# Kernel tuning notes

Hardware: AMD Instinct MI355X
Metric: run time of the kernel (lower is better)

Reference implementation:

```python
import jax, jax.numpy as jnp
import numpy as np

N_CELLS = 100000
CHANNELS = 64
NNZ = 1600000


def _spmm(rows, cols, vals, x, n):
    # y[i] = sum_{k: rows[k]==i} vals[k] * x[cols[k]]  -- sparse Laplacian matvec over features
    return jax.ops.segment_sum(vals[:, None] * x[cols], rows, num_segments=n)


def setup_inputs() -> dict:
    key = jax.random.key(0)
    ks = jax.random.split(key, 9)
    scale = 1.0 / np.sqrt(CHANNELS)
    return {
        "x": jax.random.normal(ks[0], (N_CELLS, CHANNELS), dtype=jnp.float32),
        "down_rows": jax.random.randint(ks[1], (NNZ,), 0, N_CELLS, dtype=jnp.int32),
        "down_cols": jax.random.randint(ks[2], (NNZ,), 0, N_CELLS, dtype=jnp.int32),
        "down_vals": jax.random.normal(ks[3], (NNZ,), dtype=jnp.float32),
        "up_rows": jax.random.randint(ks[4], (NNZ,), 0, N_CELLS, dtype=jnp.int32),
        "up_cols": jax.random.randint(ks[5], (NNZ,), 0, N_CELLS, dtype=jnp.int32),
        "up_vals": jax.random.normal(ks[6], (NNZ,), dtype=jnp.float32),
        "w_conv": jax.random.normal(ks[7], (CHANNELS, CHANNELS), dtype=jnp.float32) * scale,
        "w_lin": jax.random.normal(ks[8], (CHANNELS, CHANNELS), dtype=jnp.float32) * scale,
    }


def reference(x, down_rows, down_cols, down_vals, up_rows, up_cols, up_vals, w_conv, w_lin):
    n = x.shape[0]
    xw = x @ w_conv  # shared Conv weight for both Laplacian paths
    x_down = _spmm(down_rows, down_cols, down_vals, xw, n)  # L_down @ (x W_conv)
    x_up = _spmm(up_rows, up_cols, up_vals, xw, n)          # L_up   @ (x W_conv)
    x_id = x @ w_lin                                         # bias-free Linear
    # Aggregation(update_func='sigmoid'): sum messages then activate
    return jax.nn.sigmoid(x_down + x_up + x_id)
```

## Files before the change

kernel.cpp:

```cpp
#include <hip/hip_runtime.h>
#include <hip/hip_bf16.h>
#include <hip/hip_fp16.h>

#define CH 64
#define RPB 128
#define RPB_SH 7
#define MAXNB 800
#define NGRP 8
#define SUBCAP 600
#define CAPG (NGRP * SUBCAP)
#define BATCH 3072
#define SPILLMAX 16384
#define FILL_BLOCKS 521
#define GEMM_PHYS 503
#define NVB (GEMM_PHYS * 2)

typedef __attribute__((ext_vector_type(8))) _Float16 half8;
typedef __attribute__((ext_vector_type(4))) float f32x4;

#define COLOFF_MASK 0x00FFFF80

__global__ __launch_bounds__(512) void gemm_fill_kernel(
    const float* __restrict__ x, const float* __restrict__ wc,
    const float* __restrict__ wl, __half* __restrict__ xwh,
    float* __restrict__ out, int n,
    const int* __restrict__ r1, const int* __restrict__ c1, const float* __restrict__ v1,
    const int* __restrict__ r2, const int* __restrict__ c2, const float* __restrict__ v2,
    int* __restrict__ gcur, int* __restrict__ spillcnt, int4* __restrict__ spill,
    int2* __restrict__ ebuf, int nnz, int nb) {
  __shared__ int2 stash[BATCH];
  __shared__ unsigned short sbuck[BATCH];
  __shared__ int hist[MAXNB];
  __shared__ int rbase[MAXNB];

  const int tid = threadIdx.x;

  if (blockIdx.x < (unsigned)FILL_BLOCKS) {
    const int grp = (int)(blockIdx.x & (NGRP - 1));
    const int tot = 2 * nnz;
    const int nbatches = (tot + BATCH - 1) / BATCH;
    for (int bt = blockIdx.x; bt < nbatches; bt += FILL_BLOCKS) {
      for (int i = tid; i < nb; i += 512) hist[i] = 0;
      __syncthreads();

      const int e0 = bt * BATCH;
      const int m = min(BATCH, tot - e0);
      for (int i = tid; i < m; i += 512) {
        const int e = e0 + i;
        int r, c;
        float v;
        if (e < nnz) {
          r = r1[e]; c = c1[e]; v = v1[e];
        } else {
          r = r2[e - nnz]; c = c2[e - nnz]; v = v2[e - nnz];
        }
        const int b = r >> RPB_SH;
        stash[i] = make_int2(((r & (RPB - 1)) << 24) | (c << 7), __float_as_int(v));
        sbuck[i] = (unsigned short)b;
        atomicAdd(&hist[b], 1);
      }
      __syncthreads();

      for (int b = tid; b < nb; b += 512) {
        const int c = hist[b];
        rbase[b] = c ? atomicAdd(&gcur[grp * nb + b], c) : 0;
        hist[b] = 0;
      }
      __syncthreads();

      for (int i = tid; i < m; i += 512) {
        const int b = sbuck[i];
        const int2 rec = stash[i];
        const int p = rbase[b] + atomicAdd(&hist[b], 1);
        if (p < SUBCAP) {
          ebuf[(size_t)b * CAPG + grp * SUBCAP + p] = rec;
        } else {
          const int sp = atomicAdd(spillcnt, 1);
          if (sp < SPILLMAX)
            spill[sp] = make_int4(b * RPB + (rec.x >> 24), rec.x & COLOFF_MASK,
                                  rec.y, 0);
        }
      }
      __syncthreads();
    }
    return;
  }

  const int vb = (int)(blockIdx.x - FILL_BLOCKS) * 2 + (tid >> 8);
  const int t256 = tid & 255;
  const int lane = t256 & 63;
  const int wv = t256 >> 6;
  const int mat = wv >> 1;
  const int tile = wv & 1;
  const float* __restrict__ W = mat ? wl : wc;

  const int i16 = lane & 15;
  const int kseg = lane >> 4;

  half8 bhi[4][2], blo[4][2];
#pragma unroll
  for (int nt = 0; nt < 4; ++nt)
#pragma unroll
    for (int kk = 0; kk < 2; ++kk)
#pragma unroll
      for (int j = 0; j < 8; ++j) {
        const float w = W[(kk * 32 + kseg * 8 + j) * CH + nt * 16 + i16];
        const _Float16 hh = (_Float16)w;
        bhi[nt][kk][j] = hh;
        blo[nt][kk][j] = (_Float16)(w - (float)hh);
      }

  const int ngroups = (n + 31) >> 5;
  for (int g = vb; g < ngroups; g += NVB) {
    const int base = g * 32 + tile * 16;
    const int row = base + i16;
    const int rowc = (row < n) ? row : (n - 1);
    const float* xp = x + (size_t)rowc * CH + kseg * 8;

    float af[16];
    {
      const float4 p0 = *(const float4*)(xp);
      const float4 p1 = *(const float4*)(xp + 4);
      const float4 q0 = *(const float4*)(xp + 32);
      const float4 q1 = *(const float4*)(xp + 36);
      af[0] = p0.x; af[1] = p0.y; af[2] = p0.z; af[3] = p0.w;
      af[4] = p1.x; af[5] = p1.y; af[6] = p1.z; af[7] = p1.w;
      af[8] = q0.x; af[9] = q0.y; af[10] = q0.z; af[11] = q0.w;
      af[12] = q1.x; af[13] = q1.y; af[14] = q1.z; af[15] = q1.w;
    }
    half8 ahi[2], alo[2];
#pragma unroll
    for (int kk = 0; kk < 2; ++kk)
#pragma unroll
      for (int j = 0; j < 8; ++j) {
        const float f = af[kk * 8 + j];
        const _Float16 hh = (_Float16)f;
        ahi[kk][j] = hh;
        alo[kk][j] = (_Float16)(f - (float)hh);
      }

    f32x4 acc[4];
#pragma unroll
    for (int nt = 0; nt < 4; ++nt) {
      f32x4 a = {0.f, 0.f, 0.f, 0.f};
#pragma unroll
      for (int kk = 0; kk < 2; ++kk) {
        a = __builtin_amdgcn_mfma_f32_16x16x32_f16(ahi[kk], bhi[nt][kk], a, 0, 0, 0);
        a = __builtin_amdgcn_mfma_f32_16x16x32_f16(alo[kk], bhi[nt][kk], a, 0, 0, 0);
        a = __builtin_amdgcn_mfma_f32_16x16x32_f16(ahi[kk], blo[nt][kk], a, 0, 0, 0);
      }
      acc[nt] = a;
    }

    if (mat == 0) {
#pragma unroll
      for (int nt = 0; nt < 4; ++nt)
#pragma unroll
        for (int r = 0; r < 4; ++r) {
          const int orow = base + kseg * 4 + r;
          if (orow < n)
            xwh[(size_t)orow * CH + nt * 16 + i16] = __float2half(acc[nt][r]);
        }
    } else {
#pragma unroll
      for (int nt = 0; nt < 4; ++nt)
#pragma unroll
        for (int r = 0; r < 4; ++r) {
          const int orow = base + kseg * 4 + r;
          if (orow < n)
            out[(size_t)orow * CH + nt * 16 + i16] = acc[nt][r];
        }
    }
  }
}

union U8 {
  uint4 u4;
  __half h[8];
};

__device__ __forceinline__ void edge_fma(float* a, const U8& u, float v) {
#pragma unroll
  for (int k = 0; k < 8; ++k)
    a[k] = fmaf(v, __half2float(u.h[k]), a[k]);
}

#define PERG 2

__global__ __launch_bounds__(512, 8) void sortgather2_kernel(
    const int* __restrict__ gcur, const int2* __restrict__ ebuf,
    const char* __restrict__ xwbytes, float4* __restrict__ outf4,
    const int* __restrict__ spillcnt, const int4* __restrict__ spill,
    int n, int nb) {
  __shared__ int2 raw[CAPG];
  __shared__ int hist[RPB];
  __shared__ int rowstart[RPB];
  __shared__ int cur[RPB];
  const int tid = threadIdx.x;
  const int b = blockIdx.x;
  const int beg = b * CAPG;

  if (tid < RPB) hist[tid] = 0;
  __syncthreads();

  int2 myrec[NGRP * PERG];
#pragma unroll
  for (int g = 0; g < NGRP; ++g) {
    const int cg = min(gcur[g * nb + b], SUBCAP);
#pragma unroll
    for (int j = 0; j < PERG; ++j) {
      const int i = j * 512 + tid;
      const bool ok = i < cg;
      int2 rec = ok ? ebuf[beg + g * SUBCAP + i] : make_int2(-1, 0);
      myrec[g * PERG + j] = rec;
      if (ok) atomicAdd(&hist[rec.x >> 24], 1);
    }
  }
  __syncthreads();

  int v = 0;
  if (tid < RPB) {
    v = hist[tid];
    cur[tid] = v;
  }
  __syncthreads();
  for (int off = 1; off < RPB; off <<= 1) {
    int t = 0;
    if (tid < RPB && tid >= off) t = cur[tid - off];
    __syncthreads();
    if (tid < RPB) cur[tid] += t;
    __syncthreads();
  }
  if (tid < RPB) {
    rowstart[tid] = cur[tid] - v;
    cur[tid] = cur[tid] - v;
  }
  __syncthreads();

#pragma unroll
  for (int g = 0; g < NGRP; ++g)
#pragma unroll
    for (int j = 0; j < PERG; ++j) {
      const int2 rec = myrec[g * PERG + j];
      if (rec.x >= 0) {
        const int pos = atomicAdd(&cur[rec.x >> 24], 1);
        raw[pos] = rec;
      }
    }
  __syncthreads();

  const int lane = tid & 63;
  const int g8 = lane >> 3;
  const int l8 = lane & 7;
  const int l8b = l8 << 4;
  const int wv = tid >> 6;
  const int sc = min(*spillcnt, SPILLMAX);

  for (int rl = wv; rl < RPB; rl += 8) {
    const int row = b * RPB + rl;
    if (row >= n) continue;

    float a[8];
#pragma unroll
    for (int k = 0; k < 8; ++k) a[k] = 0.f;

    const int rbeg = rowstart[rl];
    const int rend = rbeg + hist[rl];

    int e = rbeg;
    for (; e + 32 <= rend; e += 32) {
      int2 rc[4];
      U8 u[4];
#pragma unroll
      for (int q = 0; q < 4; ++q) rc[q] = raw[e + q * 8 + g8];
#pragma unroll
      for (int q = 0; q < 4; ++q)
        u[q].u4 = *(const uint4*)(xwbytes + (rc[q].x & COLOFF_MASK) + l8b);
#pragma unroll
      for (int q = 0; q < 4; ++q) edge_fma(a, u[q], __int_as_float(rc[q].y));
    }
    for (; e + 16 <= rend; e += 16) {
      const int2 rc0 = raw[e + g8];
      const int2 rc1 = raw[e + 8 + g8];
      U8 u0, u1;
      u0.u4 = *(const uint4*)(xwbytes + (rc0.x & COLOFF_MASK) + l8b);
      u1.u4 = *(const uint4*)(xwbytes + (rc1.x & COLOFF_MASK) + l8b);
      edge_fma(a, u0, __int_as_float(rc0.y));
      edge_fma(a, u1, __int_as_float(rc1.y));
    }
    for (; e < rend; e += 8) {
      const int idx = e + g8;
      const bool ok = idx < rend;
      const int2 rc = raw[ok ? idx : (rend - 1)];
      U8 u;
      u.u4 = *(const uint4*)(xwbytes + (rc.x & COLOFF_MASK) + l8b);
      edge_fma(a, u, ok ? __int_as_float(rc.y) : 0.f);
    }

    if (sc > 0) {
      for (int s = 0; s < sc; ++s) {
        const int4 r = spill[s];
        if (r.x == row && g8 == 0) {
          U8 u;
          u.u4 = *(const uint4*)(xwbytes + r.y + l8b);
          edge_fma(a, u, __int_as_float(r.z));
        }
      }
    }

#pragma unroll
    for (int k = 0; k < 8; ++k) {
      a[k] += __shfl_xor(a[k], 8, 64);
      a[k] += __shfl_xor(a[k], 16, 64);
      a[k] += __shfl_xor(a[k], 32, 64);
    }

    if (lane < 8) {
      const float4 lin0 = outf4[(size_t)row * 16 + 2 * l8];
      const float4 lin1 = outf4[(size_t)row * 16 + 2 * l8 + 1];
      float4 o0, o1;
      o0.x = 1.f / (1.f + __expf(-(lin0.x + a[0])));
      o0.y = 1.f / (1.f + __expf(-(lin0.y + a[1])));
      o0.z = 1.f / (1.f + __expf(-(lin0.z + a[2])));
      o0.w = 1.f / (1.f + __expf(-(lin0.w + a[3])));
      o1.x = 1.f / (1.f + __expf(-(lin1.x + a[4])));
      o1.y = 1.f / (1.f + __expf(-(lin1.y + a[5])));
      o1.z = 1.f / (1.f + __expf(-(lin1.z + a[6])));
      o1.w = 1.f / (1.f + __expf(-(lin1.w + a[7])));
      outf4[(size_t)row * 16 + 2 * l8] = o0;
      outf4[(size_t)row * 16 + 2 * l8 + 1] = o1;
    }
  }
}

__global__ __launch_bounds__(256) void gemm_kernel(
    const float* __restrict__ x, const float* __restrict__ wc,
    const float* __restrict__ wl, __half* __restrict__ xwh,
    float* __restrict__ out, int n) {
  const int lane = threadIdx.x & 63;
  const int wv = threadIdx.x >> 6;
  const int mat = wv >> 1;
  const int tile = wv & 1;
  const float* __restrict__ W = mat ? wl : wc;
  const int i16 = lane & 15;
  const int kseg = lane >> 4;

  half8 bhi[4][2], blo[4][2];
#pragma unroll
  for (int nt = 0; nt < 4; ++nt)
#pragma unroll
    for (int kk = 0; kk < 2; ++kk)
#pragma unroll
      for (int j = 0; j < 8; ++j) {
        const float w = W[(kk * 32 + kseg * 8 + j) * CH + nt * 16 + i16];
        const _Float16 hh = (_Float16)w;
        bhi[nt][kk][j] = hh;
        blo[nt][kk][j] = (_Float16)(w - (float)hh);
      }

  const int ngroups = (n + 31) >> 5;
  for (int g = blockIdx.x; g < ngroups; g += gridDim.x) {
    const int base = g * 32 + tile * 16;
    const int row = base + i16;
    const int rowc = (row < n) ? row : (n - 1);
    const float* xp = x + (size_t)rowc * CH + kseg * 8;
    float af[16];
    {
      const float4 p0 = *(const float4*)(xp);
      const float4 p1 = *(const float4*)(xp + 4);
      const float4 q0 = *(const float4*)(xp + 32);
      const float4 q1 = *(const float4*)(xp + 36);
      af[0] = p0.x; af[1] = p0.y; af[2] = p0.z; af[3] = p0.w;
      af[4] = p1.x; af[5] = p1.y; af[6] = p1.z; af[7] = p1.w;
      af[8] = q0.x; af[9] = q0.y; af[10] = q0.z; af[11] = q0.w;
      af[12] = q1.x; af[13] = q1.y; af[14] = q1.z; af[15] = q1.w;
    }
    half8 ahi[2], alo[2];
#pragma unroll
    for (int kk = 0; kk < 2; ++kk)
#pragma unroll
      for (int j = 0; j < 8; ++j) {
        const float f = af[kk * 8 + j];
        const _Float16 hh = (_Float16)f;
        ahi[kk][j] = hh;
        alo[kk][j] = (_Float16)(f - (float)hh);
      }
    f32x4 acc[4];
#pragma unroll
    for (int nt = 0; nt < 4; ++nt) {
      f32x4 a = {0.f, 0.f, 0.f, 0.f};
#pragma unroll
      for (int kk = 0; kk < 2; ++kk) {
        a = __builtin_amdgcn_mfma_f32_16x16x32_f16(ahi[kk], bhi[nt][kk], a, 0, 0, 0);
        a = __builtin_amdgcn_mfma_f32_16x16x32_f16(alo[kk], bhi[nt][kk], a, 0, 0, 0);
        a = __builtin_amdgcn_mfma_f32_16x16x32_f16(ahi[kk], blo[nt][kk], a, 0, 0, 0);
      }
      acc[nt] = a;
    }
    if (mat == 0) {
#pragma unroll
      for (int nt = 0; nt < 4; ++nt)
#pragma unroll
        for (int r = 0; r < 4; ++r) {
          const int orow = base + kseg * 4 + r;
          if (orow < n)
            xwh[(size_t)orow * CH + nt * 16 + i16] = __float2half(acc[nt][r]);
        }
    } else {
#pragma unroll
      for (int nt = 0; nt < 4; ++nt)
#pragma unroll
        for (int r = 0; r < 4; ++r) {
          const int orow = base + kseg * 4 + r;
          if (orow < n)
            out[(size_t)orow * CH + nt * 16 + i16] = acc[nt][r];
        }
    }
  }
}

__global__ __launch_bounds__(256) void scatter_kernel(
    const int* __restrict__ rows, const int* __restrict__ cols,
    const float* __restrict__ vals, const __half* __restrict__ xwh,
    float* __restrict__ out, int nnz) {
  const int lane = threadIdx.x & 63;
  const int wid = (blockIdx.x * blockDim.x + threadIdx.x) >> 6;
  const int nwaves = (gridDim.x * blockDim.x) >> 6;
  for (int k = wid; k < nnz; k += nwaves) {
    const float xv = __half2float(xwh[(size_t)cols[k] * CH + lane]);
    atomicAdd(&out[(size_t)rows[k] * CH + lane], vals[k] * xv);
  }
}

__global__ __launch_bounds__(256) void sigmoid_kernel(float* __restrict__ out, int n4) {
  const int i = blockIdx.x * blockDim.x + threadIdx.x;
  if (i < n4) {
    float4 v = reinterpret_cast<float4*>(out)[i];
    v.x = 1.f / (1.f + __expf(-v.x));
    v.y = 1.f / (1.f + __expf(-v.y));
    v.z = 1.f / (1.f + __expf(-v.z));
    v.w = 1.f / (1.f + __expf(-v.w));
    reinterpret_cast<float4*>(out)[i] = v;
  }
}

extern "C" void kernel_launch(void* const* d_in, const int* in_sizes, int n_in,
                              void* d_out, int out_size, void* d_ws, size_t ws_size,
                              hipStream_t stream) {
  const float* x         = (const float*)d_in[0];
  const int*   down_rows = (const int*)d_in[1];
  const int*   down_cols = (const int*)d_in[2];
  const float* down_vals = (const float*)d_in[3];
  const int*   up_rows   = (const int*)d_in[4];
  const int*   up_cols   = (const int*)d_in[5];
  const float* up_vals   = (const float*)d_in[6];
  const float* w_conv    = (const float*)d_in[7];
  const float* w_lin     = (const float*)d_in[8];

  const int n   = in_sizes[0] / CH;
  const int nnz = in_sizes[1];
  const int nb  = (n + RPB - 1) / RPB;

  float* out = (float*)d_out;

  char* p = (char*)d_ws;
  __half* xwh  = (__half*)p;  p += (size_t)n * CH * 2;
  int* gcur    = (int*)p;  p += (size_t)NGRP * nb * 4;
  int* spillc  = (int*)p;  p += 16;
  p = (char*)(((uintptr_t)p + 15) & ~(uintptr_t)15);
  int4* spill  = (int4*)p; p += (size_t)SPILLMAX * 16;
  int2* ebuf   = (int2*)p; p += (size_t)nb * CAPG * 8;
  const size_t need = (size_t)(p - (char*)d_ws);

  if (ws_size >= need && nb <= MAXNB && n < (1 << 17)) {
    (void)hipMemsetAsync(gcur, 0, (size_t)NGRP * nb * 4 + 16, stream);
    gemm_fill_kernel<<<FILL_BLOCKS + GEMM_PHYS, 512, 0, stream>>>(
        x, w_conv, w_lin, xwh, out, n,
        down_rows, down_cols, down_vals, up_rows, up_cols, up_vals,
        gcur, spillc, spill, ebuf, nnz, nb);
    sortgather2_kernel<<<nb, 512, 0, stream>>>(
        gcur, ebuf, (const char*)xwh, (float4*)out, spillc, spill, n, nb);
  } else {
    gemm_kernel<<<1024, 256, 0, stream>>>(x, w_conv, w_lin, xwh, out, n);
    scatter_kernel<<<4096, 256, 0, stream>>>(down_rows, down_cols, down_vals, xwh, out, nnz);
    scatter_kernel<<<4096, 256, 0, stream>>>(up_rows, up_cols, up_vals, xwh, out, nnz);
    const int n4 = (n * CH) / 4;
    sigmoid_kernel<<<(n4 + 255) / 256, 256, 0, stream>>>(out, n4);
  }
}
```

Baseline: 123.8 us.

## Split each sort-gather bucket across two half-row blocks to cut LDS footprint

The sort-gather kernel now launches two 256-thread blocks per 128-row bucket, each handling 64 rows and staging only its own edges in a smaller shared buffer (HCAP records instead of the full bucket capacity). Each block reads the bucket's edge list twice from global memory, once for the histogram and once for the placement, rather than holding the records in registers. The goal is lower shared-memory and register use per block, so more blocks can be resident and more gathers are in flight. In exchange the edge buffer is read twice per half, and a slow fallback path rescans the global edge list whenever a half overflows the smaller buffer.

```diff
diff --git a/kernel.cpp b/kernel.cpp
--- a/kernel.cpp
+++ b/kernel.cpp
@@ -5,10 +5,12 @@
 #define CH 64
 #define RPB 128
 #define RPB_SH 7
+#define HROWS 64
 #define MAXNB 800
 #define NGRP 8
 #define SUBCAP 600
 #define CAPG (NGRP * SUBCAP)
+#define HCAP 2368
 #define BATCH 3072
 #define SPILLMAX 16384
 #define FILL_BLOCKS 521
@@ -185,68 +187,76 @@
     a[k] = fmaf(v, __half2float(u.h[k]), a[k]);
 }
 
-#define PERG 2
-
-__global__ __launch_bounds__(512, 8) void sortgather2_kernel(
+__global__ __launch_bounds__(256, 8) void sortgather3_kernel(
     const int* __restrict__ gcur, const int2* __restrict__ ebuf,
     const char* __restrict__ xwbytes, float4* __restrict__ outf4,
     const int* __restrict__ spillcnt, const int4* __restrict__ spill,
     int n, int nb) {
-  __shared__ int2 raw[CAPG];
-  __shared__ int hist[RPB];
-  __shared__ int rowstart[RPB];
-  __shared__ int cur[RPB];
+  __shared__ int2 raw[HCAP];
+  __shared__ int hist[HROWS];
+  __shared__ int rowstart[HROWS];
+  __shared__ int cur[HROWS];
+  __shared__ int ovf;
   const int tid = threadIdx.x;
-  const int b = blockIdx.x;
+  const int b = (int)(blockIdx.x >> 1);
+  const int h = (int)(blockIdx.x & 1);
   const int beg = b * CAPG;
-
-  if (tid < RPB) hist[tid] = 0;
+  const int hbase = h << 6;
+
+  if (tid < HROWS) hist[tid] = 0;
+  if (tid == 0) ovf = 0;
   __syncthreads();
 
-  int2 myrec[NGRP * PERG];
+  int gsz[NGRP];
+#pragma unroll
+  for (int g = 0; g < NGRP; ++g) gsz[g] = min(gcur[g * nb + b], SUBCAP);
+
 #pragma unroll
   for (int g = 0; g < NGRP; ++g) {
-    const int cg = min(gcur[g * nb + b], SUBCAP);
-#pragma unroll
-    for (int j = 0; j < PERG; ++j) {
-      const int i = j * 512 + tid;
-      const bool ok = i < cg;
-      int2 rec = ok ? ebuf[beg + g * SUBCAP + i] : make_int2(-1, 0);
-      myrec[g * PERG + j] = rec;
-      if (ok) atomicAdd(&hist[rec.x >> 24], 1);
+    const int cg = gsz[g];
+    for (int i = tid; i < cg; i += 256) {
+      const int lr = ebuf[beg + g * SUBCAP + i].x >> 24;
+      if ((lr >> 6) == h) atomicAdd(&hist[lr & 63], 1);
     }
   }
   __syncthreads();
 
   int v = 0;
-  if (tid < RPB) {
+  if (tid < HROWS) {
     v = hist[tid];
     cur[tid] = v;
   }
   __syncthreads();
-  for (int off = 1; off < RPB; off <<= 1) {
+  for (int off = 1; off < HROWS; off <<= 1) {
     int t = 0;
-    if (tid < RPB && tid >= off) t = cur[tid - off];
+    if (tid < HROWS && tid >= off) t = cur[tid - off];
     __syncthreads();
-    if (tid < RPB) cur[tid] += t;
+    if (tid < HROWS) cur[tid] += t;
     __syncthreads();
   }
-  if (tid < RPB) {
+  if (tid < HROWS) {
     rowstart[tid] = cur[tid] - v;
     cur[tid] = cur[tid] - v;
+    if (tid == HROWS - 1 && cur[tid] + v > HCAP) ovf = 1;
   }
   __syncthreads();
 
-#pragma unroll
-  for (int g = 0; g < NGRP; ++g)
-#pragma unroll
-    for (int j = 0; j < PERG; ++j) {
-      const int2 rec = myrec[g * PERG + j];
-      if (rec.x >= 0) {
-        const int pos = atomicAdd(&cur[rec.x >> 24], 1);
-        raw[pos] = rec;
-      }
-    }
+  const bool fallback = (ovf != 0);
+
+  if (!fallback) {
+#pragma unroll
+    for (int g = 0; g < NGRP; ++g) {
+      const int cg = gsz[g];
+      for (int i = tid; i < cg; i += 256) {
+        const int2 rec = ebuf[beg + g * SUBCAP + i];
+        const int lr = rec.x >> 24;
+        if ((lr >> 6) == h) {
+          const int pos = atomicAdd(&cur[lr & 63], 1);
+          if (pos < HCAP) raw[pos] = rec;
+        }
+      }
+    }
+  }
   __syncthreads();
 
   const int lane = tid & 63;
@@ -256,45 +266,62 @@
   const int wv = tid >> 6;
   const int sc = min(*spillcnt, SPILLMAX);
 
-  for (int rl = wv; rl < RPB; rl += 8) {
-    const int row = b * RPB + rl;
+  for (int rl = wv; rl < HROWS; rl += 4) {
+    const int row = b * RPB + hbase + rl;
     if (row >= n) continue;
 
     float a[8];
 #pragma unroll
     for (int k = 0; k < 8; ++k) a[k] = 0.f;
 
-    const int rbeg = rowstart[rl];
-    const int rend = rbeg + hist[rl];
-
-    int e = rbeg;
-    for (; e + 32 <= rend; e += 32) {
-      int2 rc[4];
-      U8 u[4];
-#pragma unroll
-      for (int q = 0; q < 4; ++q) rc[q] = raw[e + q * 8 + g8];
-#pragma unroll
-      for (int q = 0; q < 4; ++q)
-        u[q].u4 = *(const uint4*)(xwbytes + (rc[q].x & COLOFF_MASK) + l8b);
-#pragma unroll
-      for (int q = 0; q < 4; ++q) edge_fma(a, u[q], __int_as_float(rc[q].y));
-    }
-    for (; e + 16 <= rend; e += 16) {
-      const int2 rc0 = raw[e + g8];
-      const int2 rc1 = raw[e + 8 + g8];
-      U8 u0, u1;
-      u0.u4 = *(const uint4*)(xwbytes + (rc0.x & COLOFF_MASK) + l8b);
-      u1.u4 = *(const uint4*)(xwbytes + (rc1.x & COLOFF_MASK) + l8b);
-      edge_fma(a, u0, __int_as_float(rc0.y));
-      edge_fma(a, u1, __int_as_float(rc1.y));
-    }
-    for (; e < rend; e += 8) {
-      const int idx = e + g8;
-      const bool ok = idx < rend;
-      const int2 rc = raw[ok ? idx : (rend - 1)];
-      U8 u;
-      u.u4 = *(const uint4*)(xwbytes + (rc.x & COLOFF_MASK) + l8b);
-      edge_fma(a, u, ok ? __int_as_float(rc.y) : 0.f);
+    if (!fallback) {
+      const int rbeg = rowstart[rl];
+      const int rend = rbeg + hist[rl];
+      int e = rbeg;
+      for (; e + 32 <= rend; e += 32) {
+        int2 rc[4];
+        U8 u[4];
+#pragma unroll
+        for (int q = 0; q < 4; ++q) rc[q] = raw[e + q * 8 + g8];
+#pragma unroll
+        for (int q = 0; q < 4; ++q)
+          u[q].u4 = *(const uint4*)(xwbytes + (rc[q].x & COLOFF_MASK) + l8b);
+#pragma unroll
+        for (int q = 0; q < 4; ++q) edge_fma(a, u[q], __int_as_float(rc[q].y));
+      }
+      for (; e + 16 <= rend; e += 16) {
+        const int2 rc0 = raw[e + g8];
+        const int2 rc1 = raw[e + 8 + g8];
+        U8 u0, u1;
+        u0.u4 = *(const uint4*)(xwbytes + (rc0.x & COLOFF_MASK) + l8b);
+        u1.u4 = *(const uint4*)(xwbytes + (rc1.x & COLOFF_MASK) + l8b);
+        edge_fma(a, u0, __int_as_float(rc0.y));
+        edge_fma(a, u1, __int_as_float(rc1.y));
+      }
+      for (; e < rend; e += 8) {
+        const int idx = e + g8;
+        const bool ok = idx < rend;
+        const int2 rc = raw[ok ? idx : (rend - 1)];
+        U8 u;
+        u.u4 = *(const uint4*)(xwbytes + (rc.x & COLOFF_MASK) + l8b);
+        edge_fma(a, u, ok ? __int_as_float(rc.y) : 0.f);
+      }
+    } else {
+      const int myLr = hbase + rl;
+#pragma unroll
+      for (int g = 0; g < NGRP; ++g) {
+        const int cg = gsz[g];
+        for (int i = 0; i < cg; i += 8) {
+          const int idx = i + g8;
+          const bool ok = idx < cg;
+          const int2 rc = ebuf[beg + g * SUBCAP + (ok ? idx : 0)];
+          if (ok && (rc.x >> 24) == myLr) {
+            U8 u;
+            u.u4 = *(const uint4*)(xwbytes + (rc.x & COLOFF_MASK) + l8b);
+            edge_fma(a, u, __int_as_float(rc.y));
+          }
+        }
+      }
     }
 
     if (sc > 0) {
@@ -478,7 +505,7 @@
         x, w_conv, w_lin, xwh, out, n,
         down_rows, down_cols, down_vals, up_rows, up_cols, up_vals,
         gcur, spillc, spill, ebuf, nnz, nb);
-    sortgather2_kernel<<<nb, 512, 0, stream>>>(
+    sortgather3_kernel<<<nb * 2, 256, 0, stream>>>(
         gcur, ebuf, (const char*)xwh, (float4*)out, spillc, spill, n, nb);
   } else {
     gemm_kernel<<<1024, 256, 0, stream>>>(x, w_conv, w_lin, xwh, out, n);
```

Measured after the change: 129.6 us. 1.05x slower.
